# Kernel optimization log

Hardware: AMD Instinct MI355X
Metric: run time of the kernel (lower is better)

The kernel has to match this reference:

```python
import jax, jax.numpy as jnp
import numpy as np

B, N, D, H = 2, 2048, 1024, 16
HD = D // H
SCALE = HD ** -0.5


def setup_inputs() -> dict:
    key = jax.random.key(0)
    ks = jax.random.split(key, 5)
    s = D ** -0.5  # keep activations well-scaled like torch Linear init
    return {
        "x": jax.random.normal(ks[0], (B, N, D), jnp.float32),
        "Wq": jax.random.normal(ks[1], (D, D), jnp.float32) * s,
        "bq": jnp.zeros((D,), jnp.float32),
        "Wk": jax.random.normal(ks[2], (D, D), jnp.float32) * s,
        "bk": jnp.zeros((D,), jnp.float32),
        "Wv": jax.random.normal(ks[3], (D, D), jnp.float32) * s,
        "bv": jnp.zeros((D,), jnp.float32),
        "Wo": jax.random.normal(ks[4], (D, D), jnp.float32) * s,
        "bo": jnp.zeros((D,), jnp.float32),
    }


def reference(x, Wq, bq, Wk, bk, Wv, bv, Wo, bo):
    # projections: [B,N,D] -> [B,H,N,HD]
    def split_heads(t):
        return t.reshape(B, N, H, HD).transpose(0, 2, 1, 3)

    q = split_heads(x @ Wq + bq)
    k = split_heads(x @ Wk + bk)
    v = split_heads(x @ Wv + bv)
    # eager attention: explicit [B,H,N,N] scores, matching the torch module
    attn = jnp.einsum("bhnd,bhmd->bhnm", q, k) * SCALE
    attn = jax.nn.softmax(attn, axis=-1)
    out = jnp.einsum("bhnm,bhmd->bhnd", attn, v)
    out = out.transpose(0, 2, 1, 3).reshape(B, N, D)
    return out @ Wo + bo
```

## Files before the change

### kernel.cpp

```cpp
#include <hip/hip_runtime.h>
#include <hip/hip_bf16.h>

typedef __attribute__((ext_vector_type(8))) short bf16x8;
typedef __attribute__((ext_vector_type(4))) float f32x4;
typedef __attribute__((ext_vector_type(4))) unsigned short us4;
typedef __attribute__((ext_vector_type(8))) unsigned short us8;
typedef unsigned short u16;

#define NB 2
#define NSEQ 2048
#define DM 1024
#define NH 16
#define HD 64
#define NTOK (NB*NSEQ)
#define QK_SCALE (0.125f * 1.4426950408889634f)

__device__ __forceinline__ u16 f2b(float f) {
  __hip_bfloat16 h = __float2bfloat16(f);
  return __builtin_bit_cast(u16, h);
}

__device__ __forceinline__ unsigned cvtpk(float a, float b) {
  unsigned r;
  asm("v_cvt_pk_bf16_f32 %0, %1, %2" : "=v"(r) : "v"(a), "v"(b));
  return r;
}

__device__ __forceinline__ void gload16(const void* g, void* l) {
  __builtin_amdgcn_global_load_lds((__attribute__((address_space(1))) void*)g,
                                   (__attribute__((address_space(3))) void*)l, 16, 0, 0);
}

__global__ __launch_bounds__(256) void k_prep(const float* __restrict__ x, u16* __restrict__ xb,
                                              const float* __restrict__ W0, const float* __restrict__ W1,
                                              const float* __restrict__ W2, const float* __restrict__ W3,
                                              u16* __restrict__ T0, u16* __restrict__ T1,
                                              u16* __restrict__ T2, u16* __restrict__ T3) {
  __shared__ float tile[64][68];
  const int bid = blockIdx.x;
  if (bid >= 1024) {
    const int idx = ((bid - 1024) * 256 + threadIdx.x) * 8;
    const float4 v0 = *(const float4*)(x + idx);
    const float4 v1 = *(const float4*)(x + idx + 4);
    us8 o;
    o[0]=f2b(v0.x); o[1]=f2b(v0.y); o[2]=f2b(v0.z); o[3]=f2b(v0.w);
    o[4]=f2b(v1.x); o[5]=f2b(v1.y); o[6]=f2b(v1.z); o[7]=f2b(v1.w);
    *(us8*)(xb + idx) = o;
    return;
  }
  const int bz = bid >> 8, by = (bid >> 4) & 15, bx = bid & 15;
  const float* W = (bz == 0) ? W0 : (bz == 1) ? W1 : (bz == 2) ? W2 : W3;
  u16* WT = (bz == 0) ? T0 : (bz == 1) ? T1 : (bz == 2) ? T2 : T3;
  const int n0 = bx * 64, k0 = by * 64;
  const int tr = threadIdx.x >> 4, tc = (threadIdx.x & 15) * 4;
#pragma unroll
  for (int rr = 0; rr < 4; ++rr) {
    const int r = rr * 16 + tr;
    *(float4*)&tile[r][tc] = *(const float4*)&W[(size_t)(k0 + r) * DM + n0 + tc];
  }
  __syncthreads();
#pragma unroll
  for (int rr = 0; rr < 4; ++rr) {
    const int nr = rr * 16 + tr;
    us4 o;
#pragma unroll
    for (int e = 0; e < 4; ++e) o[e] = f2b(tile[tc + e][nr]);
    *(us4*)&WT[(size_t)(n0 + nr) * DM + k0 + tc] = o;
  }
}

__global__ __launch_bounds__(256) void k_gemm_qkv(
    const u16* __restrict__ xb,
    const u16* __restrict__ WqT, const u16* __restrict__ WkT, const u16* __restrict__ WvT,
    const float* __restrict__ bq, const float* __restrict__ bk, const float* __restrict__ bv,
    u16* __restrict__ Qb, u16* __restrict__ Kb, u16* __restrict__ Vtb)
{
  const int z = blockIdx.z;
  const bool isV = (z == 2);
  const u16* Ap = (z == 0) ? WqT : (z == 1) ? WkT : xb;
  const u16* Bt = isV ? WvT : xb;
  const float* bp = (z == 0) ? bq : (z == 1) ? bk : bv;
  const float scale = (z == 0) ? QK_SCALE : 1.0f;
  u16* outp = (z == 0) ? Qb : (z == 1) ? Kb : Vtb;
  const int i0 = isV ? blockIdx.x * 128 : blockIdx.y * 128;
  const int j0 = isV ? blockIdx.y * 128 : blockIdx.x * 128;

  __shared__ char smem[32 * 1024];
  const int tid = threadIdx.x, lane = tid & 63, wv = tid >> 6;
  const int li = lane & 15, g = lane >> 4;
  const int wi = wv >> 1, wj = wv & 1;

  f32x4 acc[4][4];
#pragma unroll
  for (int a = 0; a < 4; ++a)
#pragma unroll
    for (int b = 0; b < 4; ++b) acc[a][b] = f32x4{0.f, 0.f, 0.f, 0.f};

  auto stage = [&](int kt, int buf) {
#pragma unroll
    for (int c = 0; c < 2; ++c) {
      const int lg = c * 256 + tid;
      const int r = lg >> 2, ch = (lg & 3) ^ (r & 3);
      gload16(Ap + (size_t)(i0 + r) * 1024 + kt * 32 + ch * 8,
              smem + buf * 16384 + lg * 16);
      gload16(Bt + (size_t)(j0 + r) * 1024 + kt * 32 + ch * 8,
              smem + buf * 16384 + 8192 + lg * 16);
    }
  };

  stage(0, 0);

  for (int kt = 0; kt < 32; ++kt) {
    __syncthreads();
    if (kt + 1 < 32) stage(kt + 1, (kt + 1) & 1);
    const char* As = smem + (kt & 1) * 16384;
    const char* Bs = As + 8192;
    bf16x8 af[4], bfr[4];
#pragma unroll
    for (int it = 0; it < 4; ++it) {
      const int ri = 64 * wi + 16 * it + li;
      af[it] = *(const bf16x8*)(As + ri * 64 + ((g * 16) ^ ((ri & 3) << 4)));
      const int rj = 64 * wj + 16 * it + li;
      bfr[it] = *(const bf16x8*)(Bs + rj * 64 + ((g * 16) ^ ((rj & 3) << 4)));
    }
#pragma unroll
    for (int it = 0; it < 4; ++it)
#pragma unroll
      for (int jt = 0; jt < 4; ++jt)
        acc[it][jt] = __builtin_amdgcn_mfma_f32_16x16x32_bf16(af[it], bfr[jt], acc[it][jt], 0, 0, 0);
  }

#pragma unroll
  for (int it = 0; it < 4; ++it) {
    const int ib = i0 + 64 * wi + 16 * it + 4 * g;
    f32x4 b4;
    if (!isV) b4 = *(const f32x4*)(bp + ib);
#pragma unroll
    for (int jt = 0; jt < 4; ++jt) {
      const int j = j0 + 64 * wj + 16 * jt + li;
      f32x4 v = acc[it][jt];
      if (!isV) {
        v += b4;
        v *= scale;
        us4 pk; pk[0]=f2b(v[0]); pk[1]=f2b(v[1]); pk[2]=f2b(v[2]); pk[3]=f2b(v[3]);
        *(us4*)(outp + (size_t)j * 1024 + ib) = pk;
      } else {
        const float bj = bp[j];
        v[0] += bj; v[1] += bj; v[2] += bj; v[3] += bj;
        us4 pk; pk[0]=f2b(v[0]); pk[1]=f2b(v[1]); pk[2]=f2b(v[2]); pk[3]=f2b(v[3]);
        const size_t addr = ((size_t)(ib >> 11) * 1024 + j) * 2048 + (ib & 2047);
        *(us4*)(outp + addr) = pk;
      }
    }
  }
}

__global__ __launch_bounds__(256) void k_gemm_out(
    const u16* __restrict__ A, const u16* __restrict__ Bt, const float* __restrict__ bias,
    float* __restrict__ outp)
{
  __shared__ char smem[48 * 1024];
  const int tid = threadIdx.x, lane = tid & 63, wv = tid >> 6;
  const int li = lane & 15, g = lane >> 4;
  const int i0 = blockIdx.y * 128, j0 = blockIdx.x * 64;

  f32x4 acc[2][4];
#pragma unroll
  for (int a = 0; a < 2; ++a)
#pragma unroll
    for (int b = 0; b < 4; ++b) acc[a][b] = f32x4{0.f, 0.f, 0.f, 0.f};

  auto stage = [&](int kt, int buf) {
#pragma unroll
    for (int c = 0; c < 4; ++c) {
      const int lg = c * 256 + tid;
      const int r = lg >> 3, ch = (lg & 7) ^ (r & 7);
      gload16(A + (size_t)(i0 + r) * 1024 + kt * 64 + ch * 8,
              smem + buf * 24576 + lg * 16);
    }
#pragma unroll
    for (int c = 0; c < 2; ++c) {
      const int lg = c * 256 + tid;
      const int r = lg >> 3, ch = (lg & 7) ^ (r & 7);
      gload16(Bt + (size_t)(j0 + r) * 1024 + kt * 64 + ch * 8,
              smem + buf * 24576 + 16384 + lg * 16);
    }
  };

  stage(0, 0);

  for (int kt = 0; kt < 16; ++kt) {
    __syncthreads();
    if (kt + 1 < 16) stage(kt + 1, (kt + 1) & 1);
    const char* As = smem + (kt & 1) * 24576;
    const char* Bs = As + 16384;
#pragma unroll
    for (int ks = 0; ks < 2; ++ks) {
      bf16x8 af[2], bfr[4];
#pragma unroll
      for (int it = 0; it < 2; ++it) {
        const int ri = 32 * wv + 16 * it + li;
        af[it] = *(const bf16x8*)(As + ri * 128 + ((ks * 64 + g * 16) ^ ((ri & 7) << 4)));
      }
#pragma unroll
      for (int jt = 0; jt < 4; ++jt) {
        const int rj = 16 * jt + li;
        bfr[jt] = *(const bf16x8*)(Bs + rj * 128 + ((ks * 64 + g * 16) ^ ((rj & 7) << 4)));
      }
#pragma unroll
      for (int it = 0; it < 2; ++it)
#pragma unroll
        for (int jt = 0; jt < 4; ++jt)
          acc[it][jt] = __builtin_amdgcn_mfma_f32_16x16x32_bf16(af[it], bfr[jt], acc[it][jt], 0, 0, 0);
    }
  }

#pragma unroll
  for (int it = 0; it < 2; ++it) {
    const int ib = i0 + 32 * wv + 16 * it + 4 * g;
    const f32x4 b4 = *(const f32x4*)(bias + ib);
#pragma unroll
    for (int jt = 0; jt < 4; ++jt) {
      const int j = j0 + 16 * jt + li;
      f32x4 v = acc[it][jt] + b4;
      *(f32x4*)(outp + (size_t)j * 1024 + ib) = v;
    }
  }
}

__global__ __launch_bounds__(256, 2) void k_attn(const u16* __restrict__ Q, const u16* __restrict__ K,
                                                 const u16* __restrict__ Vt, u16* __restrict__ O)
{
  __shared__ char smem[64 * 1024];
  const int tid = threadIdx.x, lane = tid & 63, w = tid >> 6;
  const int li = lane & 15, g = lane >> 4;

  const int vid = blockIdx.x;
  const int u = vid >> 3;
  const int bh = (vid & 7) * 4 + (u >> 4);
  const int qt = u & 15;
  const int b = bh >> 4, h = bh & 15;
  const int n0 = qt * 128;
  const size_t tokbase = (size_t)b * NSEQ;
  const int iq = 16 * w + li;

  bf16x8 qf[2][2];
#pragma unroll
  for (int grp = 0; grp < 2; ++grp)
#pragma unroll
    for (int ks = 0; ks < 2; ++ks)
      qf[grp][ks] = *(const bf16x8*)(Q + (tokbase + n0 + 64 * grp + iq) * 1024 + h * 64 + 32 * ks + 8 * g);

  bf16x8 ones;
#pragma unroll
  for (int e = 0; e < 8; ++e) ones[e] = (short)0x3F80;

  f32x4 oacc[2][4];
#pragma unroll
  for (int grp = 0; grp < 2; ++grp)
#pragma unroll
    for (int dt = 0; dt < 4; ++dt) oacc[grp][dt] = f32x4{0.f, 0.f, 0.f, 0.f};
  f32x4 ls[2] = {f32x4{0.f,0.f,0.f,0.f}, f32x4{0.f,0.f,0.f,0.f}};

  const u16* Kb = K + tokbase * 1024 + h * 64;
  const u16* Vb = Vt + (size_t)bh * 64 * 2048;

  auto stage = [&](int t, int buf) {
    const int jn = t * 64;
#pragma unroll
    for (int c = 0; c < 2; ++c) {
      const int lg = c * 256 + tid;
      const int r = lg >> 3, ch = (lg & 7) ^ (r & 7);
      gload16(Kb + (size_t)(jn + r) * 1024 + ch * 8, smem + buf * 8192 + (c * 256 + w * 64) * 16);
      gload16(Vb + (size_t)r * 2048 + jn + ch * 8, smem + 24576 + buf * 8192 + (c * 256 + w * 64) * 16);
    }
  };

  auto body = [&](int t, int buf) {
    const char* Ks = smem + buf * 8192;
    const char* Vs = smem + 24576 + buf * 8192;

    f32x4 s[2][4];
#pragma unroll
    for (int grp = 0; grp < 2; ++grp)
#pragma unroll
      for (int jt = 0; jt < 4; ++jt) s[grp][jt] = f32x4{0.f, 0.f, 0.f, 0.f};
#pragma unroll
    for (int ks = 0; ks < 2; ++ks) {
#pragma unroll
      for (int jt = 0; jt < 4; ++jt) {
        const int rj = 16 * jt + li;
        bf16x8 a = *(const bf16x8*)(Ks + rj * 128 + ((ks * 64 + g * 16) ^ ((rj & 7) << 4)));
        s[0][jt] = __builtin_amdgcn_mfma_f32_16x16x32_bf16(a, qf[0][ks], s[0][jt], 0, 0, 0);
        s[1][jt] = __builtin_amdgcn_mfma_f32_16x16x32_bf16(a, qf[1][ks], s[1][jt], 0, 0, 0);
      }
    }

#pragma unroll
    for (int grp = 0; grp < 2; ++grp) {
      const int row = iq + 64 * grp;
      char* Pr = smem + 49152 + row * 128;
      const int swz = (row & 7) << 4;
#pragma unroll
      for (int jt = 0; jt < 4; ++jt) {
        uint2 pk;
        pk.x = cvtpk(exp2f(s[grp][jt][0]), exp2f(s[grp][jt][1]));
        pk.y = cvtpk(exp2f(s[grp][jt][2]), exp2f(s[grp][jt][3]));
        *(uint2*)(Pr + ((32 * jt + 8 * g) ^ swz)) = pk;
      }
    }

#pragma unroll
    for (int ks = 0; ks < 2; ++ks) {
      const int kb = ks * 64 + g * 16;
      bf16x8 bpv0 = *(const bf16x8*)(smem + 49152 + iq * 128 + (kb ^ ((iq & 7) << 4)));
      bf16x8 bpv1 = *(const bf16x8*)(smem + 49152 + (iq + 64) * 128 + (kb ^ ((iq & 7) << 4)));
      ls[0] = __builtin_amdgcn_mfma_f32_16x16x32_bf16(ones, bpv0, ls[0], 0, 0, 0);
      ls[1] = __builtin_amdgcn_mfma_f32_16x16x32_bf16(ones, bpv1, ls[1], 0, 0, 0);
#pragma unroll
      for (int dt = 0; dt < 4; ++dt) {
        const int rd = 16 * dt + li;
        bf16x8 av = *(const bf16x8*)(Vs + rd * 128 + (kb ^ ((rd & 7) << 4)));
        oacc[0][dt] = __builtin_amdgcn_mfma_f32_16x16x32_bf16(av, bpv0, oacc[0][dt], 0, 0, 0);
        oacc[1][dt] = __builtin_amdgcn_mfma_f32_16x16x32_bf16(av, bpv1, oacc[1][dt], 0, 0, 0);
      }
    }
  };

  stage(0, 0);
  stage(1, 1);

#pragma unroll 1
  for (int tt = 0; tt < 10; ++tt) {
#pragma unroll
    for (int uu = 0; uu < 3; ++uu) {
      const int t = tt * 3 + uu;
      asm volatile("s_waitcnt vmcnt(4)" ::: "memory");
      __builtin_amdgcn_s_barrier();
      stage(t + 2, (uu + 2) % 3);
      body(t, uu);
    }
  }
  asm volatile("s_waitcnt vmcnt(4)" ::: "memory");
  __builtin_amdgcn_s_barrier();
  body(30, 0);
  asm volatile("s_waitcnt vmcnt(0)" ::: "memory");
  __builtin_amdgcn_s_barrier();
  body(31, 1);

#pragma unroll
  for (int grp = 0; grp < 2; ++grp) {
    const float inv = 1.f / ls[grp][0];
    const size_t obase = (tokbase + n0 + 64 * grp + iq) * 1024 + h * 64;
#pragma unroll
    for (int dt = 0; dt < 4; ++dt) {
      us4 pk;
#pragma unroll
      for (int e = 0; e < 4; ++e) pk[e] = f2b(oacc[grp][dt][e] * inv);
      *(us4*)(O + obase + 16 * dt + 4 * g) = pk;
    }
  }
}

extern "C" void kernel_launch(void* const* d_in, const int* in_sizes, int n_in,
                              void* d_out, int out_size, void* d_ws, size_t ws_size,
                              hipStream_t stream) {
  const float* x  = (const float*)d_in[0];
  const float* Wq = (const float*)d_in[1];
  const float* bq = (const float*)d_in[2];
  const float* Wk = (const float*)d_in[3];
  const float* bk = (const float*)d_in[4];
  const float* Wv = (const float*)d_in[5];
  const float* bv = (const float*)d_in[6];
  const float* Wo = (const float*)d_in[7];
  const float* bo = (const float*)d_in[8];

  char* ws = (char*)d_ws;
  u16* xb  = (u16*)(ws);
  u16* WqT = (u16*)(ws + (8  << 20));
  u16* WkT = (u16*)(ws + (10 << 20));
  u16* WvT = (u16*)(ws + (12 << 20));
  u16* WoT = (u16*)(ws + (14 << 20));
  u16* Qb  = (u16*)(ws + (16 << 20));
  u16* Kb  = (u16*)(ws + (24 << 20));
  u16* Vtb = (u16*)(ws + (32 << 20));
  u16* Ob  = (u16*)(ws + (40 << 20));

  k_prep<<<3072, 256, 0, stream>>>(x, xb, Wq, Wk, Wv, Wo, WqT, WkT, WvT, WoT);

  k_gemm_qkv<<<dim3(32, 8, 3), 256, 0, stream>>>(xb, WqT, WkT, WvT, bq, bk, bv, Qb, Kb, Vtb);

  k_attn<<<512, 256, 0, stream>>>(Qb, Kb, Vtb, Ob);

  k_gemm_out<<<dim3(64, 8), 256, 0, stream>>>(WoT, Ob, bo, (float*)d_out);
}
```

Baseline: 118.0 us.

## Shrink attention tiles to 64 queries and 32 keys for higher occupancy

The attention kernel now processes 64 query rows per block instead of 128, and streams 32-key tiles instead of 64. This cuts shared memory to about 29KB and raises launch bounds to 4 blocks per CU, with twice as many blocks in the grid. The loop schedule, LDS layout and swizzles for K, V and P are reworked to match, and sched_barriers are added around the syncs. The aim is better latency hiding through more resident waves. The cost is less K/V reuse per block, twice the global K/V traffic, and more barriers per unit of work.

```diff
diff --git a/kernel.cpp b/kernel.cpp
--- a/kernel.cpp
+++ b/kernel.cpp
@@ -228,102 +228,91 @@
   }
 }
 
-__global__ __launch_bounds__(256, 2) void k_attn(const u16* __restrict__ Q, const u16* __restrict__ K,
+__global__ __launch_bounds__(256, 4) void k_attn(const u16* __restrict__ Q, const u16* __restrict__ K,
                                                  const u16* __restrict__ Vt, u16* __restrict__ O)
 {
-  __shared__ char smem[64 * 1024];
+  __shared__ char smem[29696];
   const int tid = threadIdx.x, lane = tid & 63, w = tid >> 6;
   const int li = lane & 15, g = lane >> 4;
 
   const int vid = blockIdx.x;
   const int u = vid >> 3;
-  const int bh = (vid & 7) * 4 + (u >> 4);
-  const int qt = u & 15;
+  const int bh = (vid & 7) * 4 + (u >> 5);
+  const int qt = u & 31;
   const int b = bh >> 4, h = bh & 15;
-  const int n0 = qt * 128;
+  const int n0 = qt * 64;
   const size_t tokbase = (size_t)b * NSEQ;
-  const int iq = 16 * w + li;
-
-  bf16x8 qf[2][2];
-#pragma unroll
-  for (int grp = 0; grp < 2; ++grp)
-#pragma unroll
-    for (int ks = 0; ks < 2; ++ks)
-      qf[grp][ks] = *(const bf16x8*)(Q + (tokbase + n0 + 64 * grp + iq) * 1024 + h * 64 + 32 * ks + 8 * g);
+  const int ql = 16 * w + li;
+
+  bf16x8 qf[2];
+#pragma unroll
+  for (int ks = 0; ks < 2; ++ks)
+    qf[ks] = *(const bf16x8*)(Q + (tokbase + n0 + ql) * 1024 + h * 64 + 32 * ks + 8 * g);
 
   bf16x8 ones;
 #pragma unroll
   for (int e = 0; e < 8; ++e) ones[e] = (short)0x3F80;
 
-  f32x4 oacc[2][4];
-#pragma unroll
-  for (int grp = 0; grp < 2; ++grp)
-#pragma unroll
-    for (int dt = 0; dt < 4; ++dt) oacc[grp][dt] = f32x4{0.f, 0.f, 0.f, 0.f};
-  f32x4 ls[2] = {f32x4{0.f,0.f,0.f,0.f}, f32x4{0.f,0.f,0.f,0.f}};
+  f32x4 oacc[4];
+#pragma unroll
+  for (int dt = 0; dt < 4; ++dt) oacc[dt] = f32x4{0.f, 0.f, 0.f, 0.f};
+  f32x4 ls = f32x4{0.f, 0.f, 0.f, 0.f};
 
   const u16* Kb = K + tokbase * 1024 + h * 64;
   const u16* Vb = Vt + (size_t)bh * 64 * 2048;
 
   auto stage = [&](int t, int buf) {
-    const int jn = t * 64;
-#pragma unroll
-    for (int c = 0; c < 2; ++c) {
-      const int lg = c * 256 + tid;
-      const int r = lg >> 3, ch = (lg & 7) ^ (r & 7);
-      gload16(Kb + (size_t)(jn + r) * 1024 + ch * 8, smem + buf * 8192 + (c * 256 + w * 64) * 16);
-      gload16(Vb + (size_t)r * 2048 + jn + ch * 8, smem + 24576 + buf * 8192 + (c * 256 + w * 64) * 16);
-    }
-  };
-
-  auto body = [&](int t, int buf) {
-    const char* Ks = smem + buf * 8192;
-    const char* Vs = smem + 24576 + buf * 8192;
-
-    f32x4 s[2][4];
-#pragma unroll
-    for (int grp = 0; grp < 2; ++grp)
-#pragma unroll
-      for (int jt = 0; jt < 4; ++jt) s[grp][jt] = f32x4{0.f, 0.f, 0.f, 0.f};
+    const int jn = t * 32;
+    {
+      const int r = tid >> 3, ch = (tid & 7) ^ (r & 7);
+      gload16(Kb + (size_t)(jn + r) * 1024 + ch * 8, smem + buf * 4096 + w * 1024);
+    }
+    {
+      const int r = tid >> 2, ch = (tid & 3) ^ (r & 3);
+      gload16(Vb + (size_t)r * 2048 + jn + ch * 8, smem + 12288 + buf * 4096 + w * 1024);
+    }
+  };
+
+  auto sync2 = [&]() {
+    asm volatile("s_waitcnt vmcnt(2)" ::: "memory");
+    __builtin_amdgcn_sched_barrier(0);
+    __builtin_amdgcn_s_barrier();
+    __builtin_amdgcn_sched_barrier(0);
+  };
+
+  auto body = [&](int buf) {
+    const char* Ks = smem + buf * 4096;
+    const char* Vs = smem + 12288 + buf * 4096;
+    char* Pr = smem + 24576 + ql * 80;
+
+    f32x4 s[2];
+    s[0] = f32x4{0.f, 0.f, 0.f, 0.f};
+    s[1] = f32x4{0.f, 0.f, 0.f, 0.f};
 #pragma unroll
     for (int ks = 0; ks < 2; ++ks) {
 #pragma unroll
-      for (int jt = 0; jt < 4; ++jt) {
+      for (int jt = 0; jt < 2; ++jt) {
         const int rj = 16 * jt + li;
         bf16x8 a = *(const bf16x8*)(Ks + rj * 128 + ((ks * 64 + g * 16) ^ ((rj & 7) << 4)));
-        s[0][jt] = __builtin_amdgcn_mfma_f32_16x16x32_bf16(a, qf[0][ks], s[0][jt], 0, 0, 0);
-        s[1][jt] = __builtin_amdgcn_mfma_f32_16x16x32_bf16(a, qf[1][ks], s[1][jt], 0, 0, 0);
+        s[jt] = __builtin_amdgcn_mfma_f32_16x16x32_bf16(a, qf[ks], s[jt], 0, 0, 0);
       }
     }
 
 #pragma unroll
-    for (int grp = 0; grp < 2; ++grp) {
-      const int row = iq + 64 * grp;
-      char* Pr = smem + 49152 + row * 128;
-      const int swz = (row & 7) << 4;
-#pragma unroll
-      for (int jt = 0; jt < 4; ++jt) {
-        uint2 pk;
-        pk.x = cvtpk(exp2f(s[grp][jt][0]), exp2f(s[grp][jt][1]));
-        pk.y = cvtpk(exp2f(s[grp][jt][2]), exp2f(s[grp][jt][3]));
-        *(uint2*)(Pr + ((32 * jt + 8 * g) ^ swz)) = pk;
-      }
-    }
-
-#pragma unroll
-    for (int ks = 0; ks < 2; ++ks) {
-      const int kb = ks * 64 + g * 16;
-      bf16x8 bpv0 = *(const bf16x8*)(smem + 49152 + iq * 128 + (kb ^ ((iq & 7) << 4)));
-      bf16x8 bpv1 = *(const bf16x8*)(smem + 49152 + (iq + 64) * 128 + (kb ^ ((iq & 7) << 4)));
-      ls[0] = __builtin_amdgcn_mfma_f32_16x16x32_bf16(ones, bpv0, ls[0], 0, 0, 0);
-      ls[1] = __builtin_amdgcn_mfma_f32_16x16x32_bf16(ones, bpv1, ls[1], 0, 0, 0);
-#pragma unroll
-      for (int dt = 0; dt < 4; ++dt) {
-        const int rd = 16 * dt + li;
-        bf16x8 av = *(const bf16x8*)(Vs + rd * 128 + (kb ^ ((rd & 7) << 4)));
-        oacc[0][dt] = __builtin_amdgcn_mfma_f32_16x16x32_bf16(av, bpv0, oacc[0][dt], 0, 0, 0);
-        oacc[1][dt] = __builtin_amdgcn_mfma_f32_16x16x32_bf16(av, bpv1, oacc[1][dt], 0, 0, 0);
-      }
+    for (int jt = 0; jt < 2; ++jt) {
+      uint2 pk;
+      pk.x = cvtpk(exp2f(s[jt][0]), exp2f(s[jt][1]));
+      pk.y = cvtpk(exp2f(s[jt][2]), exp2f(s[jt][3]));
+      *(uint2*)(Pr + 32 * jt + 8 * g) = pk;
+    }
+
+    bf16x8 bpv = *(const bf16x8*)(Pr + 16 * g);
+    ls = __builtin_amdgcn_mfma_f32_16x16x32_bf16(ones, bpv, ls, 0, 0, 0);
+#pragma unroll
+    for (int dt = 0; dt < 4; ++dt) {
+      const int rd = 16 * dt + li;
+      bf16x8 av = *(const bf16x8*)(Vs + rd * 64 + ((16 * g) ^ ((rd & 3) << 4)));
+      oacc[dt] = __builtin_amdgcn_mfma_f32_16x16x32_bf16(av, bpv, oacc[dt], 0, 0, 0);
     }
   };
 
@@ -331,34 +320,37 @@
   stage(1, 1);
 
 #pragma unroll 1
-  for (int tt = 0; tt < 10; ++tt) {
+  for (int tt = 0; tt < 20; ++tt) {
 #pragma unroll
     for (int uu = 0; uu < 3; ++uu) {
       const int t = tt * 3 + uu;
-      asm volatile("s_waitcnt vmcnt(4)" ::: "memory");
-      __builtin_amdgcn_s_barrier();
+      sync2();
       stage(t + 2, (uu + 2) % 3);
-      body(t, uu);
-    }
-  }
-  asm volatile("s_waitcnt vmcnt(4)" ::: "memory");
+      body(uu);
+    }
+  }
+  sync2();
+  stage(62, 2);
+  body(0);
+  sync2();
+  stage(63, 0);
+  body(1);
+  sync2();
+  body(2);
+  asm volatile("s_waitcnt vmcnt(0)" ::: "memory");
+  __builtin_amdgcn_sched_barrier(0);
   __builtin_amdgcn_s_barrier();
-  body(30, 0);
-  asm volatile("s_waitcnt vmcnt(0)" ::: "memory");
-  __builtin_amdgcn_s_barrier();
-  body(31, 1);
-
-#pragma unroll
-  for (int grp = 0; grp < 2; ++grp) {
-    const float inv = 1.f / ls[grp][0];
-    const size_t obase = (tokbase + n0 + 64 * grp + iq) * 1024 + h * 64;
-#pragma unroll
-    for (int dt = 0; dt < 4; ++dt) {
-      us4 pk;
-#pragma unroll
-      for (int e = 0; e < 4; ++e) pk[e] = f2b(oacc[grp][dt][e] * inv);
-      *(us4*)(O + obase + 16 * dt + 4 * g) = pk;
-    }
+  __builtin_amdgcn_sched_barrier(0);
+  body(0);
+
+  const float inv = 1.f / ls[0];
+  const size_t obase = (tokbase + n0 + ql) * 1024 + h * 64;
+#pragma unroll
+  for (int dt = 0; dt < 4; ++dt) {
+    us4 pk;
+#pragma unroll
+    for (int e = 0; e < 4; ++e) pk[e] = f2b(oacc[dt][e] * inv);
+    *(us4*)(O + obase + 16 * dt + 4 * g) = pk;
   }
 }
 
@@ -390,7 +382,7 @@
 
   k_gemm_qkv<<<dim3(32, 8, 3), 256, 0, stream>>>(xb, WqT, WkT, WvT, bq, bk, bv, Qb, Kb, Vtb);
 
-  k_attn<<<512, 256, 0, stream>>>(Qb, Kb, Vtb, Ob);
+  k_attn<<<1024, 256, 0, stream>>>(Qb, Kb, Vtb, Ob);
 
   k_gemm_out<<<dim3(64, 8), 256, 0, stream>>>(WoT, Ob, bo, (float*)d_out);
 }
```

Result: slower. 124.5 us (+5.4%).
